# Optimization experiments

Measured on AMD Instinct MI355X. Metric: run time of the kernel, lower is better.

The kernel has to match this reference:

```python
import jax, jax.numpy as jnp
import numpy as np

D_MODEL, D_STATE, D_CONV, EXPAND = 1024, 16, 4, 2
D_INNER = EXPAND * D_MODEL            # 2048
DT_RANK = D_MODEL // 16               # 64
B, L = 2, 4096


def setup_inputs() -> dict:
    key = jax.random.key(0)
    ks = jax.random.split(key, 8)
    s = 0.02
    u = jax.random.normal(ks[0], (B, L, D_MODEL), jnp.float32)
    in_proj_w = jax.random.normal(ks[1], (2 * D_INNER, D_MODEL), jnp.float32) * s
    conv_w = jax.random.normal(ks[2], (D_INNER, D_CONV), jnp.float32) * 0.2
    conv_b = jnp.zeros((D_INNER,), jnp.float32)
    x_proj_w = jax.random.normal(ks[3], (DT_RANK + 2 * D_STATE, D_INNER), jnp.float32) * s
    dt_proj_w = jax.random.normal(ks[4], (D_INNER, DT_RANK), jnp.float32) * (DT_RANK ** -0.5)
    # dt bias initialized so softplus(dt_bias) in [1e-3, 1e-1], as in mamba-ssm
    dt = jnp.exp(jax.random.uniform(ks[5], (D_INNER,)) * (np.log(0.1) - np.log(1e-3)) + np.log(1e-3))
    dt_bias = jnp.log(-jnp.expm1(-dt) * jnp.exp(dt))  # inverse softplus
    A_log = jnp.log(jnp.tile(jnp.arange(1, D_STATE + 1, dtype=jnp.float32), (D_INNER, 1)))
    D_in = jnp.ones((D_INNER,), jnp.float32)
    out_proj_w = jax.random.normal(ks[6], (D_MODEL, D_INNER), jnp.float32) * s
    D_skip = jnp.ones((D_MODEL,), jnp.float32)
    return dict(u=u, in_proj_w=in_proj_w, conv_w=conv_w, conv_b=conv_b,
                x_proj_w=x_proj_w, dt_proj_w=dt_proj_w, dt_bias=dt_bias,
                A_log=A_log, D_in=D_in, out_proj_w=out_proj_w, D_skip=D_skip)


def _mamba(u, in_proj_w, conv_w, conv_b, x_proj_w, dt_proj_w, dt_bias,
           A_log, D_in, out_proj_w):
    b, l, _ = u.shape
    xz = jnp.einsum('bld,ed->ble', u, in_proj_w)      # (B,L,2*Din)
    x, z = jnp.split(xz, 2, axis=-1)
    # causal depthwise conv1d over time, kernel size D_CONV
    xp = jnp.pad(x, ((0, 0), (D_CONV - 1, 0), (0, 0)))
    x = sum(xp[:, k:k + l, :] * conv_w[:, k] for k in range(D_CONV)) + conv_b
    x = jax.nn.silu(x)
    x_dbl = jnp.einsum('bld,ed->ble', x, x_proj_w)    # (B,L,dt_rank+2N)
    dt = jax.nn.softplus(x_dbl[..., :DT_RANK] @ dt_proj_w.T + dt_bias)  # (B,L,Din)
    Bm = x_dbl[..., DT_RANK:DT_RANK + D_STATE]        # (B,L,N)
    Cm = x_dbl[..., DT_RANK + D_STATE:]               # (B,L,N)
    A = -jnp.exp(A_log)                               # (Din,N)

    def step(h, inp):
        dt_t, B_t, C_t, x_t = inp                     # (B,Din),(B,N),(B,N),(B,Din)
        dA = jnp.exp(dt_t[..., None] * A)             # (B,Din,N)
        h = dA * h + (dt_t * x_t)[..., None] * B_t[:, None, :]
        y = jnp.einsum('bdn,bn->bd', h, C_t)
        return h, y

    h0 = jnp.zeros((b, D_INNER, D_STATE), u.dtype)
    xs = (dt.transpose(1, 0, 2), Bm.transpose(1, 0, 2),
          Cm.transpose(1, 0, 2), x.transpose(1, 0, 2))
    _, ys = jax.lax.scan(step, h0, xs)                # (L,B,Din)
    y = ys.transpose(1, 0, 2) + x * D_in
    y = y * jax.nn.silu(z)
    return jnp.einsum('bld,ed->ble', y, out_proj_w)   # (B,L,D_MODEL)


def reference(u, in_proj_w, conv_w, conv_b, x_proj_w, dt_proj_w, dt_bias,
              A_log, D_in, out_proj_w, D_skip):
    y = _mamba(u, in_proj_w, conv_w, conv_b, x_proj_w, dt_proj_w, dt_bias,
               A_log, D_in, out_proj_w)
    return y + D_skip[None, None, :] * u
```

## Files before the change

kernel.cpp:

```cpp
#include <hip/hip_runtime.h>

typedef unsigned short u16;
typedef unsigned int u32;
typedef __attribute__((ext_vector_type(8))) short s16x8;
typedef __attribute__((ext_vector_type(4))) float f32x4;

__device__ inline u16 f2bf(float f){
    u32 u = __float_as_uint(f);
    u32 r = (u + 0x7fffu + ((u >> 16) & 1u)) >> 16;
    return (u16)r;
}
__device__ inline float bf2f(u16 h){
    return __uint_as_float(((u32)h) << 16);
}

#define GLOAD_LDS16(g, l) __builtin_amdgcn_global_load_lds( \
    (__attribute__((address_space(1))) void*)(void*)(g),    \
    (__attribute__((address_space(3))) void*)(l), 16, 0, 0)

#define MEMFENCE asm volatile("" ::: "memory")

__global__ __launch_bounds__(512, 2) void gemm256_in(
    const u16* __restrict__ A, const u16* __restrict__ B,
    int K, int nbn, u16* __restrict__ Cb, u16* __restrict__ Cb2)
{
    __shared__ u16 lds[2][2][256 * 64];
    const int tid  = threadIdx.x;
    const int lane = tid & 63, wave = tid >> 6;
    const int wr = wave >> 2, wc = wave & 3;
    const int l16 = lane & 15, lg = lane >> 4;

    int wgid = blockIdx.x, nwg = gridDim.x;
    int swz = wgid;
    if ((nwg & 7) == 0) { int cpx = nwg >> 3; swz = (wgid & 7) * cpx + (wgid >> 3); }
    const int bm = swz / nbn, bn = swz % nbn;

    const u16* Ab = A + (size_t)bm * 256 * K;
    const u16* Bb = B + (size_t)bn * 256 * K;

    const int srow   = wave * 8 + (lane >> 3);
    const int scol16 = (lane & 7) ^ ((lane >> 3) & 7);

    auto stageA = [&](int buf, int kt) {
        #pragma unroll
        for (int j = 0; j < 4; j++)
            GLOAD_LDS16(Ab + (size_t)(j * 64 + srow) * K + kt + scol16 * 8,
                        &lds[buf][0][(j * 64 + wave * 8) * 64]);
    };
    auto stageB = [&](int buf, int kt) {
        #pragma unroll
        for (int j = 0; j < 4; j++)
            GLOAD_LDS16(Bb + (size_t)(j * 64 + srow) * K + kt + scol16 * 8,
                        &lds[buf][1][(j * 64 + wave * 8) * 64]);
    };

    f32x4 acc[2][2][4][2] = {};
    s16x8 a[4][2], b0[2][2], b1[2][2];

    auto readA = [&](int buf, int mh) {
        #pragma unroll
        for (int m = 0; m < 4; m++)
            #pragma unroll
            for (int ks = 0; ks < 2; ks++) {
                int row = wr * 128 + mh * 64 + m * 16 + l16;
                int c16 = (ks * 4 + lg) ^ (l16 & 7);
                a[m][ks] = *(const s16x8*)&lds[buf][0][row * 64 + c16 * 8];
            }
    };
    auto readB = [&](int buf, int nh, s16x8 (&b)[2][2]) {
        #pragma unroll
        for (int n = 0; n < 2; n++)
            #pragma unroll
            for (int ks = 0; ks < 2; ks++) {
                int row = wc * 64 + nh * 32 + n * 16 + l16;
                int c16 = (ks * 4 + lg) ^ (l16 & 7);
                b[n][ks] = *(const s16x8*)&lds[buf][1][row * 64 + c16 * 8];
            }
    };

    const int NT = K >> 6;

    stageA(0, 0); stageB(0, 0);
    asm volatile("s_waitcnt vmcnt(0)" ::: "memory");
    __builtin_amdgcn_s_barrier();
    MEMFENCE;

    for (int t = 0; t < NT; t++) {
        const int bufc = t & 1;
        const bool pre = (t < NT - 1);
        #pragma unroll
        for (int p = 0; p < 4; p++) {
            const int mh = (p >> 1) & 1;
            const int nh = (p == 0 || p == 3) ? 0 : 1;
            if (p == 0 && pre) stageA(bufc ^ 1, (t + 1) << 6);
            if (p == 1 && pre) stageB(bufc ^ 1, (t + 1) << 6);
            if (p == 0) { readA(bufc, 0); readB(bufc, 0, b0); }
            if (p == 1) { readB(bufc, 1, b1); }
            if (p == 2) { readA(bufc, 1); }
            if (p == 3 && pre)
                asm volatile("s_waitcnt vmcnt(0)" ::: "memory");
            MEMFENCE;
            __builtin_amdgcn_s_barrier();
            MEMFENCE;
            __builtin_amdgcn_s_setprio(1);
            {
                s16x8 (&bb)[2][2] = (nh == 0) ? b0 : b1;
                #pragma unroll
                for (int m = 0; m < 4; m++)
                    #pragma unroll
                    for (int n = 0; n < 2; n++)
                        #pragma unroll
                        for (int ks = 0; ks < 2; ks++)
                            acc[mh][nh][m][n] = __builtin_amdgcn_mfma_f32_16x16x32_bf16(
                                a[m][ks], bb[n][ks], acc[mh][nh][m][n], 0, 0, 0);
            }
            __builtin_amdgcn_s_setprio(0);
            if (p == 3) {
                MEMFENCE;
                __builtin_amdgcn_s_barrier();
                MEMFENCE;
            }
        }
    }

    #pragma unroll
    for (int mh = 0; mh < 2; mh++)
        #pragma unroll
        for (int nh = 0; nh < 2; nh++)
            #pragma unroll
            for (int m = 0; m < 4; m++)
                #pragma unroll
                for (int n = 0; n < 2; n++) {
                    const int col = bn * 256 + wc * 64 + nh * 32 + n * 16 + l16;
                    #pragma unroll
                    for (int r = 0; r < 4; r++) {
                        const int row = bm * 256 + wr * 128 + mh * 64 + m * 16 + lg * 4 + r;
                        float v = acc[mh][nh][m][n][r];
                        if (col < 2048) Cb[(size_t)row * 2048 + col] = f2bf(v);
                        else            Cb2[(size_t)row * 2048 + (col - 2048)] = f2bf(v);
                    }
                }
}

__global__ __launch_bounds__(256) void gemm_out(
    const u16* __restrict__ A, const u16* __restrict__ B,
    int N, int K, int nbn,
    float* __restrict__ Cf, const float* __restrict__ aux0,
    const float* __restrict__ aux1)
{
    constexpr int BK = 64;
    __shared__ u16 As[128 * BK];
    __shared__ u16 Bs[128 * BK];
    const int tid  = threadIdx.x;
    const int lane = tid & 63, wave = tid >> 6;
    const int wr = wave >> 1, wc = wave & 1;
    const int l16 = lane & 15, lg = lane >> 4;

    int wgid = blockIdx.x, nwg = gridDim.x;
    int swz = wgid;
    if ((nwg & 7) == 0) { int cpx = nwg >> 3; swz = (wgid & 7) * cpx + (wgid >> 3); }
    const int bm = swz / nbn, bn = swz % nbn;

    const u16* Ab = A + (size_t)bm * 128 * K;
    const u16* Bb = B + (size_t)bn * 128 * K;

    f32x4 acc[4][4] = {};

    for (int kt = 0; kt < K; kt += BK) {
        #pragma unroll
        for (int p = 0; p < 4; p++) {
            int flat = (p * 256 + tid) * 8;
            int r = flat >> 6, c = flat & 63;
            GLOAD_LDS16(Ab + (size_t)r * K + kt + c, As + flat);
        }
        #pragma unroll
        for (int p = 0; p < 4; p++) {
            int flat = (p * 256 + tid) * 8;
            int r = flat >> 6, c = flat & 63;
            GLOAD_LDS16(Bb + (size_t)r * K + kt + c, Bs + flat);
        }
        asm volatile("s_waitcnt vmcnt(0)" ::: "memory");
        __syncthreads();
        #pragma unroll
        for (int kk = 0; kk < 2; kk++) {
            s16x8 a[4], b[4];
            #pragma unroll
            for (int m = 0; m < 4; m++)
                a[m] = *(const s16x8*)&As[(wr * 64 + m * 16 + l16) * BK + kk * 32 + lg * 8];
            #pragma unroll
            for (int n = 0; n < 4; n++)
                b[n] = *(const s16x8*)&Bs[(wc * 64 + n * 16 + l16) * BK + kk * 32 + lg * 8];
            #pragma unroll
            for (int m = 0; m < 4; m++)
                #pragma unroll
                for (int n = 0; n < 4; n++)
                    acc[m][n] = __builtin_amdgcn_mfma_f32_16x16x32_bf16(a[m], b[n], acc[m][n], 0, 0, 0);
        }
        __syncthreads();
    }

    const int row0 = bm * 128 + wr * 64 + lg * 4;
    const int col0 = bn * 128 + wc * 64 + l16;
    #pragma unroll
    for (int m = 0; m < 4; m++)
        #pragma unroll
        for (int n = 0; n < 4; n++) {
            const int col = col0 + n * 16;
            #pragma unroll
            for (int r = 0; r < 4; r++) {
                const int row = row0 + m * 16 + r;
                float o = acc[m][n][r] + aux0[col] * aux1[(size_t)row * N + col];
                Cf[(size_t)row * N + col] = o;
            }
        }
}

__global__ __launch_bounds__(256) void gemm_dt(
    const u16* __restrict__ A, const u16* __restrict__ B,
    int M, int N, int K,
    u16* __restrict__ Cb, const float* __restrict__ aux0)
{
    constexpr int BK = 64;
    __shared__ u16 As[128 * BK];
    __shared__ u16 Bs[128 * BK];
    const int tid  = threadIdx.x;
    const int lane = tid & 63, wave = tid >> 6;
    const int wr = wave >> 1, wc = wave & 1;
    const int bm = blockIdx.x, bn = blockIdx.y;
    const int l16 = lane & 15, lg = lane >> 4;

    const u16* Ab = A + (size_t)bm * 128 * K;
    const u16* Bb = B + (size_t)bn * 128 * K;

    f32x4 acc[4][4] = {};

    for (int kt = 0; kt < K; kt += BK) {
        #pragma unroll
        for (int p = 0; p < 4; p++) {
            int flat = (p * 256 + tid) * 8;
            int r = flat >> 6, c = flat & 63;
            GLOAD_LDS16(Ab + (size_t)r * K + kt + c, As + flat);
        }
        #pragma unroll
        for (int p = 0; p < 4; p++) {
            int flat = (p * 256 + tid) * 8;
            int r = flat >> 6, c = flat & 63;
            GLOAD_LDS16(Bb + (size_t)r * K + kt + c, Bs + flat);
        }
        asm volatile("s_waitcnt vmcnt(0)" ::: "memory");
        __syncthreads();
        #pragma unroll
        for (int kk = 0; kk < 2; kk++) {
            s16x8 a[4], b[4];
            #pragma unroll
            for (int m = 0; m < 4; m++)
                a[m] = *(const s16x8*)&As[(wr * 64 + m * 16 + l16) * BK + kk * 32 + lg * 8];
            #pragma unroll
            for (int n = 0; n < 4; n++)
                b[n] = *(const s16x8*)&Bs[(wc * 64 + n * 16 + l16) * BK + kk * 32 + lg * 8];
            #pragma unroll
            for (int m = 0; m < 4; m++)
                #pragma unroll
                for (int n = 0; n < 4; n++)
                    acc[m][n] = __builtin_amdgcn_mfma_f32_16x16x32_bf16(a[m], b[n], acc[m][n], 0, 0, 0);
        }
        __syncthreads();
    }

    const int row0 = bm * 128 + wr * 64 + lg * 4;
    const int col0 = bn * 128 + wc * 64 + l16;
    #pragma unroll
    for (int m = 0; m < 4; m++)
        #pragma unroll
        for (int n = 0; n < 4; n++) {
            const int col = col0 + n * 16;
            #pragma unroll
            for (int r = 0; r < 4; r++) {
                const int row = row0 + m * 16 + r;
                float t2 = acc[m][n][r] + aux0[col];
                float sp = (t2 > 15.f) ? t2 : __logf(1.f + __expf(t2));
                Cb[(size_t)row * N + col] = f2bf(sp);
            }
        }
}

__global__ __launch_bounds__(256) void gemm_xproj_sk(
    const u16* __restrict__ A, const u16* __restrict__ B,
    float* __restrict__ part)
{
    constexpr int BK = 64, K = 2048;
    __shared__ u16 As[128 * BK];
    __shared__ u16 Bs[128 * BK];
    const int tid  = threadIdx.x;
    const int lane = tid & 63, wave = tid >> 6;
    const int wr = wave >> 1, wc = wave & 1;
    const int bm = blockIdx.x, sk = blockIdx.y;
    const int l16 = lane & 15, lg = lane >> 4;

    const u16* Ab = A + (size_t)bm * 128 * K;
    const u16* Bb = B;
    const int kt0 = sk * 256;

    f32x4 acc[4][4] = {};

    for (int kt = kt0; kt < kt0 + 256; kt += BK) {
        #pragma unroll
        for (int p = 0; p < 4; p++) {
            int flat = (p * 256 + tid) * 8;
            int r = flat >> 6, c = flat & 63;
            GLOAD_LDS16(Ab + (size_t)r * K + kt + c, As + flat);
        }
        #pragma unroll
        for (int p = 0; p < 4; p++) {
            int flat = (p * 256 + tid) * 8;
            int r = flat >> 6, c = flat & 63;
            GLOAD_LDS16(Bb + (size_t)r * K + kt + c, Bs + flat);
        }
        asm volatile("s_waitcnt vmcnt(0)" ::: "memory");
        __syncthreads();
        #pragma unroll
        for (int kk = 0; kk < 2; kk++) {
            s16x8 a[4], b[4];
            #pragma unroll
            for (int m = 0; m < 4; m++)
                a[m] = *(const s16x8*)&As[(wr * 64 + m * 16 + l16) * BK + kk * 32 + lg * 8];
            #pragma unroll
            for (int n = 0; n < 4; n++)
                b[n] = *(const s16x8*)&Bs[(wc * 64 + n * 16 + l16) * BK + kk * 32 + lg * 8];
            #pragma unroll
            for (int m = 0; m < 4; m++)
                #pragma unroll
                for (int n = 0; n < 4; n++)
                    acc[m][n] = __builtin_amdgcn_mfma_f32_16x16x32_bf16(a[m], b[n], acc[m][n], 0, 0, 0);
        }
        __syncthreads();
    }

    float* pb = part + (size_t)sk * 8192 * 128;
    const int row0 = bm * 128 + wr * 64 + lg * 4;
    const int col0 = wc * 64 + l16;
    #pragma unroll
    for (int m = 0; m < 4; m++)
        #pragma unroll
        for (int n = 0; n < 4; n++)
            #pragma unroll
            for (int r = 0; r < 4; r++)
                pb[(size_t)(row0 + m * 16 + r) * 128 + col0 + n * 16] = acc[m][n][r];
}

__global__ __launch_bounds__(256) void combine_xproj(
    const float* __restrict__ part, u16* __restrict__ dtin,
    float* __restrict__ xBC)
{
    const int gid = blockIdx.x * 256 + threadIdx.x;
    const int row = gid >> 7, col = gid & 127;
    float s = 0.f;
    #pragma unroll
    for (int sk = 0; sk < 8; sk++) s += part[(size_t)sk * 8192 * 128 + gid];
    if (col < 64)      dtin[(size_t)row * 64 + col] = f2bf(s);
    else if (col < 96) xBC[(size_t)row * 32 + (col - 64)] = s;
}

__global__ __launch_bounds__(256) void cvt_all(
    const float* __restrict__ u, const float* __restrict__ Wi,
    const float* __restrict__ Wo, const float* __restrict__ Wdt,
    const float* __restrict__ Wx,
    u16* __restrict__ u_bf, u16* __restrict__ Wi_bf, u16* __restrict__ Wo_bf,
    u16* __restrict__ Wdt_bf, u16* __restrict__ Wx_bf)
{
    size_t i = ((size_t)blockIdx.x * 256 + threadIdx.x) * 4;
    const size_t E0 = 8388608, E1 = E0 + 4194304, E2 = E1 + 2097152, E3 = E2 + 131072;
    f32x4 v;
    u16* dst;
    size_t off;
    if (i < E0)      { off = i;      v = *(const f32x4*)(u + off);   dst = u_bf + off; }
    else if (i < E1) { off = i - E0; v = *(const f32x4*)(Wi + off);  dst = Wi_bf + off; }
    else if (i < E2) { off = i - E1; v = *(const f32x4*)(Wo + off);  dst = Wo_bf + off; }
    else if (i < E3) { off = i - E2; v = *(const f32x4*)(Wdt + off); dst = Wdt_bf + off; }
    else {
        off = i - E3;
        size_t row = off >> 11;
        if (row < 96) v = *(const f32x4*)(Wx + off);
        else          v = (f32x4){0.f, 0.f, 0.f, 0.f};
        dst = Wx_bf + off;
    }
    ushort4 o;
    o.x = f2bf(v[0]); o.y = f2bf(v[1]); o.z = f2bf(v[2]); o.w = f2bf(v[3]);
    *(ushort4*)dst = o;
}

__global__ __launch_bounds__(256) void conv_silu(
    const u16* __restrict__ xzx, const float* __restrict__ cw,
    const float* __restrict__ cb, u16* __restrict__ xc)
{
    const int tid = threadIdx.x;
    const int d0 = tid * 8;
    const int t0 = blockIdx.x * 16;
    const int b  = blockIdx.y;
    float W0[8], W1[8], W2[8], W3[8], BI[8];
    #pragma unroll
    for (int j = 0; j < 8; j++) {
        f32x4 w = *(const f32x4*)(cw + (size_t)(d0 + j) * 4);
        W0[j] = w[0]; W1[j] = w[1]; W2[j] = w[2]; W3[j] = w[3];
        BI[j] = cb[d0 + j];
    }
    const u16* xp = xzx + (size_t)(b * 4096) * 2048 + d0;
    u16* op = xc + (size_t)(b * 4096) * 2048 + d0;

    float x0[8], x1[8], x2[8];
    #pragma unroll
    for (int j = 0; j < 8; j++) { x0[j] = 0.f; x1[j] = 0.f; x2[j] = 0.f; }
    if (t0 >= 3) {
        s16x8 v0 = *(const s16x8*)(xp + (size_t)(t0 - 3) * 2048);
        s16x8 v1 = *(const s16x8*)(xp + (size_t)(t0 - 2) * 2048);
        s16x8 v2 = *(const s16x8*)(xp + (size_t)(t0 - 1) * 2048);
        #pragma unroll
        for (int j = 0; j < 8; j++) {
            x0[j] = bf2f((u16)v0[j]); x1[j] = bf2f((u16)v1[j]); x2[j] = bf2f((u16)v2[j]);
        }
    }
    #pragma unroll
    for (int k = 0; k < 16; k++) {
        int t = t0 + k;
        s16x8 cv = *(const s16x8*)(xp + (size_t)t * 2048);
        s16x8 o;
        #pragma unroll
        for (int j = 0; j < 8; j++) {
            float c = bf2f((u16)cv[j]);
            float s = BI[j] + W0[j] * x0[j] + W1[j] * x1[j] + W2[j] * x2[j] + W3[j] * c;
            float v = s * __fdividef(1.f, 1.f + __expf(-s));
            o[j] = (short)f2bf(v);
            x0[j] = x1[j]; x1[j] = x2[j]; x2[j] = c;
        }
        *(s16x8*)(op + (size_t)t * 2048) = o;
    }
}

__global__ __launch_bounds__(256) void scan_p1(
    const u16* __restrict__ dtb, const u16* __restrict__ xc,
    const float* __restrict__ xBC, const float* __restrict__ A_log,
    u16* __restrict__ Aagg, u16* __restrict__ Bagg)
{
    __shared__ float Bsh[64][16];
    const int tid = threadIdx.x;
    const int d = blockIdx.x * 256 + tid;
    const int c = blockIdx.y, b = blockIdx.z;

    {
        int ti = tid >> 2, p = tid & 3;
        f32x4 bv = *(const f32x4*)(xBC + ((size_t)(b * 4096 + c * 64 + ti)) * 32 + p * 4);
        *(f32x4*)&Bsh[ti][p * 4] = bv;
    }
    __syncthreads();

    float Adn[16];
    #pragma unroll
    for (int q = 0; q < 4; q++) {
        f32x4 al = *(const f32x4*)(A_log + (size_t)d * 16 + q * 4);
        #pragma unroll
        for (int j = 0; j < 4; j++) Adn[q * 4 + j] = -__expf(al[j]);
    }

    const size_t base = (size_t)(b * 4096 + c * 64) * 2048 + d;
    const u16* dtp = dtb + base;
    const u16* xp  = xc  + base;

    float h[16];
    #pragma unroll
    for (int n = 0; n < 16; n++) h[n] = 0.f;
    float sumdt = 0.f;

    float dtv = bf2f(dtp[0]), xv = bf2f(xp[0]);
    for (int t = 0; t < 64; t++) {
        float ndt = 0.f, nx = 0.f;
        if (t < 63) { ndt = bf2f(dtp[(size_t)(t + 1) * 2048]); nx = bf2f(xp[(size_t)(t + 1) * 2048]); }
        float dtx = dtv * xv;
        sumdt += dtv;
        f32x4 B0 = *(const f32x4*)&Bsh[t][0];
        f32x4 B1 = *(const f32x4*)&Bsh[t][4];
        f32x4 B2 = *(const f32x4*)&Bsh[t][8];
        f32x4 B3 = *(const f32x4*)&Bsh[t][12];
        #pragma unroll
        for (int n = 0; n < 16; n++) {
            float Bv = (n < 4) ? B0[n] : (n < 8) ? B1[n - 4] : (n < 12) ? B2[n - 8] : B3[n - 12];
            float aa = __expf(Adn[n] * dtv);
            h[n] = fmaf(aa, h[n], dtx * Bv);
        }
        dtv = ndt; xv = nx;
    }

    const size_t abase = ((size_t)(b * 2048 + d) * 16) * 64 + c;
    #pragma unroll
    for (int n = 0; n < 16; n++) {
        Aagg[abase + (size_t)n * 64] = f2bf(__expf(Adn[n] * sumdt));
        Bagg[abase + (size_t)n * 64] = f2bf(h[n]);
    }
}

__global__ __launch_bounds__(256) void scan_p2(
    const u16* __restrict__ Aagg, u16* __restrict__ BaggH0)
{
    const int gid = blockIdx.x * 256 + threadIdx.x;
    const size_t base = (size_t)gid * 64;
    s16x8 Ar[8], Br[8];
    #pragma unroll
    for (int i = 0; i < 8; i++) {
        Ar[i] = *(const s16x8*)(Aagg + base + i * 8);
        Br[i] = *(const s16x8*)(BaggH0 + base + i * 8);
    }
    s16x8 Hr[8];
    float h = 0.f;
    #pragma unroll
    for (int i = 0; i < 8; i++) {
        #pragma unroll
        for (int j = 0; j < 8; j++) {
            float ac = bf2f((u16)Ar[i][j]);
            float bc = bf2f((u16)Br[i][j]);
            Hr[i][j] = (short)f2bf(h);
            h = fmaf(ac, h, bc);
        }
    }
    #pragma unroll
    for (int i = 0; i < 8; i++)
        *(s16x8*)(BaggH0 + base + i * 8) = Hr[i];
}

__global__ __launch_bounds__(256) void scan_p3(
    const u16* __restrict__ dtb, const u16* __restrict__ xc,
    const float* __restrict__ xBC, const float* __restrict__ A_log,
    const u16* __restrict__ H0, const u16* __restrict__ xzz,
    const float* __restrict__ D_in, u16* __restrict__ yy)
{
    __shared__ float BCs[64][32];
    const int tid = threadIdx.x;
    const int d = blockIdx.x * 256 + tid;
    const int c = blockIdx.y, b = blockIdx.z;

    {
        int ti = tid >> 2, p = tid & 3;
        const float* src = xBC + ((size_t)(b * 4096 + c * 64 + ti)) * 32 + p * 8;
        f32x4 v0 = *(const f32x4*)src;
        f32x4 v1 = *(const f32x4*)(src + 4);
        *(f32x4*)&BCs[ti][p * 8] = v0;
        *(f32x4*)&BCs[ti][p * 8 + 4] = v1;
    }
    __syncthreads();

    float Adn[16];
    #pragma unroll
    for (int q = 0; q < 4; q++) {
        f32x4 al = *(const f32x4*)(A_log + (size_t)d * 16 + q * 4);
        #pragma unroll
        for (int j = 0; j < 4; j++) Adn[q * 4 + j] = -__expf(al[j]);
    }
    const float Dd = D_in[d];

    float h[16];
    const size_t hbase = ((size_t)(b * 2048 + d) * 16) * 64 + c;
    #pragma unroll
    for (int n = 0; n < 16; n++) h[n] = bf2f(H0[hbase + (size_t)n * 64]);

    const size_t base = (size_t)(b * 4096 + c * 64) * 2048 + d;
    const u16* dtp = dtb + base;
    const u16* xp  = xc  + base;
    const u16* zp  = xzz + base;
    u16* yp = yy + base;

    float dtv = bf2f(dtp[0]), xv = bf2f(xp[0]), zv = bf2f(zp[0]);
    for (int t = 0; t < 64; t++) {
        float ndt = 0.f, nx = 0.f, nz = 0.f;
        if (t < 63) {
            ndt = bf2f(dtp[(size_t)(t + 1) * 2048]);
            nx  = bf2f(xp[(size_t)(t + 1) * 2048]);
            nz  = bf2f(zp[(size_t)(t + 1) * 2048]);
        }
        float dtx = dtv * xv;
        f32x4 B0 = *(const f32x4*)&BCs[t][0];
        f32x4 B1 = *(const f32x4*)&BCs[t][4];
        f32x4 B2 = *(const f32x4*)&BCs[t][8];
        f32x4 B3 = *(const f32x4*)&BCs[t][12];
        f32x4 C0 = *(const f32x4*)&BCs[t][16];
        f32x4 C1 = *(const f32x4*)&BCs[t][20];
        f32x4 C2 = *(const f32x4*)&BCs[t][24];
        f32x4 C3 = *(const f32x4*)&BCs[t][28];
        float y = 0.f;
        #pragma unroll
        for (int n = 0; n < 16; n++) {
            float Bv = (n < 4) ? B0[n] : (n < 8) ? B1[n - 4] : (n < 12) ? B2[n - 8] : B3[n - 12];
            float Cv = (n < 4) ? C0[n] : (n < 8) ? C1[n - 4] : (n < 12) ? C2[n - 8] : C3[n - 12];
            float aa = __expf(Adn[n] * dtv);
            h[n] = fmaf(aa, h[n], dtx * Bv);
            y = fmaf(h[n], Cv, y);
        }
        float sz = zv * __fdividef(1.f, 1.f + __expf(-zv));
        float val = fmaf(xv, Dd, y) * sz;
        yp[(size_t)t * 2048] = f2bf(val);
        dtv = ndt; xv = nx; zv = nz;
    }
}

extern "C" void kernel_launch(void* const* d_in, const int* in_sizes, int n_in,
                              void* d_out, int out_size, void* d_ws, size_t ws_size,
                              hipStream_t stream)
{
    const float* u       = (const float*)d_in[0];
    const float* Wi      = (const float*)d_in[1];
    const float* conv_w  = (const float*)d_in[2];
    const float* conv_b  = (const float*)d_in[3];
    const float* Wx      = (const float*)d_in[4];
    const float* Wdt     = (const float*)d_in[5];
    const float* dt_bias = (const float*)d_in[6];
    const float* A_log   = (const float*)d_in[7];
    const float* D_in_   = (const float*)d_in[8];
    const float* Wo      = (const float*)d_in[9];
    const float* D_skip  = (const float*)d_in[10];
    float* out = (float*)d_out;
    (void)in_sizes; (void)n_in; (void)out_size;

    const size_t MB = 1u << 20;
    char* ws = (char*)d_ws;
    u16*   xzx    = (u16*)(ws + 0);
    float* xpart  = (float*)(ws + 0);
    u16*   Aagg   = (u16*)(ws + 0);
    u16*   BaggH0 = (u16*)(ws + 8 * MB);
    u16*   xzz    = (u16*)(ws + 32 * MB);
    u16*   xc     = (u16*)(ws + 64 * MB);
    u16*   u_bf   = (u16*)(ws + 96 * MB);
    u16*   Wi_bf  = (u16*)(ws + 112 * MB);
    u16*   dtb    = (u16*)(ws + 96 * MB);
    u16*   Wx_bf  = (u16*)(ws + 128 * MB);
    u16*   Wdt_bf = (u16*)(ws + 128 * MB + 512 * 1024);
    u16*   yybuf  = (u16*)(ws + 128 * MB);
    float* xBC    = (float*)(ws + 160 * MB);
    u16*   dtin   = (u16*)(ws + 161 * MB);
    u16*   Wo_bf  = (u16*)(ws + 162 * MB);
    const size_t NEED = 166 * MB;
    if (ws_size < NEED) return;

    cvt_all<<<14720, 256, 0, stream>>>(u, Wi, Wo, Wdt, Wx,
                                       u_bf, Wi_bf, Wo_bf, Wdt_bf, Wx_bf);

    gemm256_in<<<512, 512, 0, stream>>>(u_bf, Wi_bf, 1024, 16, xzx, xzz);
    conv_silu<<<dim3(256, 2), 256, 0, stream>>>(xzx, conv_w, conv_b, xc);

    gemm_xproj_sk<<<dim3(64, 8), 256, 0, stream>>>(xc, Wx_bf, xpart);
    combine_xproj<<<4096, 256, 0, stream>>>(xpart, dtin, xBC);

    gemm_dt<<<dim3(64, 16), 256, 0, stream>>>(dtin, Wdt_bf, 8192, 2048, 64,
                                              dtb, dt_bias);

    scan_p1<<<dim3(8, 64, 2), 256, 0, stream>>>(dtb, xc, xBC, A_log, Aagg, BaggH0);
    scan_p2<<<256, 256, 0, stream>>>(Aagg, BaggH0);
    scan_p3<<<dim3(8, 64, 2), 256, 0, stream>>>(dtb, xc, xBC, A_log, BaggH0, xzz,
                                                D_in_, yybuf);

    gemm_out<<<512, 256, 0, stream>>>(yybuf, Wo_bf, 1024, 2048, 8,
                                      out, D_skip, u);
}
```

Baseline: 387.3 us.

## Pipeline in-proj GEMM with half-tile staging and reuse 256 tile for out-proj

Adds a new in-projection GEMM that stages A and B in half tiles across two K buffers. Global-to-LDS loads for the next slices are interleaved with four MFMA phases per K step, separated by barriers and priority hints, and the LDS reads use an XOR swizzle. The old 256x256 kernel is repurposed for the output projection with the skip-connection epilogue, replacing the 128x128 gemm_out. The aim is to overlap memory traffic with matrix math and to reuse more data per tile on the out-proj. In exchange, occupancy drops to 1 block per CU for the in-proj, and out-proj runs only 128 workgroups, which may underfill the GPU.

```diff
diff --git a/kernel.cpp b/kernel.cpp
--- a/kernel.cpp
+++ b/kernel.cpp
@@ -19,10 +19,145 @@
     (__attribute__((address_space(3))) void*)(l), 16, 0, 0)
 
 #define MEMFENCE asm volatile("" ::: "memory")
-
-__global__ __launch_bounds__(512, 2) void gemm256_in(
+#define BAR do { MEMFENCE; __builtin_amdgcn_s_barrier(); MEMFENCE; } while (0)
+
+__global__ __launch_bounds__(512, 1) void gemm256_pipe(
     const u16* __restrict__ A, const u16* __restrict__ B,
     int K, int nbn, u16* __restrict__ Cb, u16* __restrict__ Cb2)
+{
+    __shared__ u16 lds[2][2][2][128 * 64];
+    const int tid  = threadIdx.x;
+    const int lane = tid & 63, wave = tid >> 6;
+    const int wr = wave >> 2, wc = wave & 3;
+    const int l16 = lane & 15, lg = lane >> 4;
+
+    int wgid = blockIdx.x, nwg = gridDim.x;
+    int swz = wgid;
+    if ((nwg & 7) == 0) { int cpx = nwg >> 3; swz = (wgid & 7) * cpx + (wgid >> 3); }
+    const int bm = swz / nbn, bn = swz % nbn;
+
+    const u16* Ab = A + (size_t)bm * 256 * K;
+    const u16* Bb = B + (size_t)bn * 256 * K;
+
+    auto stage_half = [&](int kbuf, int mat, int half, int kt) {
+        const u16* src = mat ? Bb : Ab;
+        #pragma unroll
+        for (int j = 0; j < 2; j++) {
+            int slot = j * 512 + tid;
+            int r = slot >> 3, cg = slot & 7;
+            GLOAD_LDS16(src + (size_t)(half * 128 + r) * K + kt + ((cg ^ (r & 7)) << 3),
+                        &lds[kbuf][mat][half][(j * 512 + wave * 64) * 8]);
+        }
+    };
+
+    f32x4 acc[2][2][4][2] = {};
+    s16x8 a[4][2], b0[2][2], b1[2][2];
+
+    auto readA = [&](int kbuf, int mh) {
+        #pragma unroll
+        for (int m = 0; m < 4; m++)
+            #pragma unroll
+            for (int ks = 0; ks < 2; ks++) {
+                int r = mh * 64 + m * 16 + l16;
+                int cg = (ks * 4 + lg) ^ (l16 & 7);
+                a[m][ks] = *(const s16x8*)&lds[kbuf][0][wr][r * 64 + cg * 8];
+            }
+    };
+    auto readB = [&](int kbuf, int nh, s16x8 (&bb)[2][2]) {
+        #pragma unroll
+        for (int n = 0; n < 2; n++)
+            #pragma unroll
+            for (int ks = 0; ks < 2; ks++) {
+                int row = wc * 64 + nh * 32 + n * 16 + l16;
+                int half = row >> 7, r = row & 127;
+                int cg = (ks * 4 + lg) ^ (l16 & 7);
+                bb[n][ks] = *(const s16x8*)&lds[kbuf][1][half][r * 64 + cg * 8];
+            }
+    };
+    auto PH = [&](int mh, int nh, s16x8 (&bb)[2][2]) {
+        BAR;
+        __builtin_amdgcn_s_setprio(1);
+        #pragma unroll
+        for (int m = 0; m < 4; m++)
+            #pragma unroll
+            for (int n = 0; n < 2; n++)
+                #pragma unroll
+                for (int ks = 0; ks < 2; ks++)
+                    acc[mh][nh][m][n] = __builtin_amdgcn_mfma_f32_16x16x32_bf16(
+                        a[m][ks], bb[n][ks], acc[mh][nh][m][n], 0, 0, 0);
+        __builtin_amdgcn_s_setprio(0);
+        BAR;
+    };
+
+    const int NT = K >> 6;
+
+    stage_half(0, 1, 0, 0); stage_half(0, 1, 1, 0);
+    stage_half(0, 0, 0, 0); stage_half(0, 0, 1, 0);
+    stage_half(1, 1, 0, 64);
+    stage_half(1, 0, 0, 64); stage_half(1, 0, 1, 64);
+    asm volatile("s_waitcnt vmcnt(6)" ::: "memory");
+    BAR;
+
+    for (int it = 0; it < (NT >> 1); it++) {
+        const int t1k = (2 * it + 1) << 6;
+        const int t2k = (2 * it + 2) << 6;
+        const int t3k = (2 * it + 3) << 6;
+        const bool pre = (2 * it + 2) < NT;
+        readA(0, 0); readB(0, 0, b0);
+        stage_half(1, 1, 1, t1k);
+        PH(0, 0, b0);
+        readB(0, 1, b1);
+        PH(0, 1, b1);
+        readA(0, 1);
+        if (pre) stage_half(0, 1, 0, t2k);
+        PH(1, 1, b1);
+        if (pre) {
+            stage_half(0, 1, 1, t2k);
+            asm volatile("s_waitcnt vmcnt(4)" ::: "memory");
+        } else {
+            asm volatile("s_waitcnt vmcnt(0)" ::: "memory");
+        }
+        PH(1, 0, b0);
+        readA(1, 0); readB(1, 0, b0);
+        if (pre) stage_half(0, 0, 0, t2k);
+        PH(0, 0, b0);
+        readB(1, 1, b1);
+        if (pre) stage_half(0, 0, 1, t2k);
+        PH(0, 1, b1);
+        readA(1, 1);
+        if (pre) stage_half(1, 1, 0, t3k);
+        PH(1, 1, b1);
+        if (pre) {
+            stage_half(1, 0, 0, t3k); stage_half(1, 0, 1, t3k);
+            asm volatile("s_waitcnt vmcnt(6)" ::: "memory");
+        }
+        PH(1, 0, b0);
+    }
+
+    #pragma unroll
+    for (int mh = 0; mh < 2; mh++)
+        #pragma unroll
+        for (int nh = 0; nh < 2; nh++)
+            #pragma unroll
+            for (int m = 0; m < 4; m++)
+                #pragma unroll
+                for (int n = 0; n < 2; n++) {
+                    const int col = bn * 256 + wc * 64 + nh * 32 + n * 16 + l16;
+                    #pragma unroll
+                    for (int r = 0; r < 4; r++) {
+                        const int row = bm * 256 + wr * 128 + mh * 64 + m * 16 + lg * 4 + r;
+                        float v = acc[mh][nh][m][n][r];
+                        if (col < 2048) Cb[(size_t)row * 2048 + col] = f2bf(v);
+                        else            Cb2[(size_t)row * 2048 + (col - 2048)] = f2bf(v);
+                    }
+                }
+}
+
+__global__ __launch_bounds__(512, 2) void gemm256_out(
+    const u16* __restrict__ A, const u16* __restrict__ B,
+    int N, int K, int nbn,
+    float* __restrict__ Cf, const float* __restrict__ aux0,
+    const float* __restrict__ aux1)
 {
     __shared__ u16 lds[2][2][256 * 64];
     const int tid  = threadIdx.x;
@@ -135,84 +270,10 @@
                     #pragma unroll
                     for (int r = 0; r < 4; r++) {
                         const int row = bm * 256 + wr * 128 + mh * 64 + m * 16 + lg * 4 + r;
-                        float v = acc[mh][nh][m][n][r];
-                        if (col < 2048) Cb[(size_t)row * 2048 + col] = f2bf(v);
-                        else            Cb2[(size_t)row * 2048 + (col - 2048)] = f2bf(v);
+                        float o = acc[mh][nh][m][n][r] + aux0[col] * aux1[(size_t)row * N + col];
+                        Cf[(size_t)row * N + col] = o;
                     }
                 }
-}
-
-__global__ __launch_bounds__(256) void gemm_out(
-    const u16* __restrict__ A, const u16* __restrict__ B,
-    int N, int K, int nbn,
-    float* __restrict__ Cf, const float* __restrict__ aux0,
-    const float* __restrict__ aux1)
-{
-    constexpr int BK = 64;
-    __shared__ u16 As[128 * BK];
-    __shared__ u16 Bs[128 * BK];
-    const int tid  = threadIdx.x;
-    const int lane = tid & 63, wave = tid >> 6;
-    const int wr = wave >> 1, wc = wave & 1;
-    const int l16 = lane & 15, lg = lane >> 4;
-
-    int wgid = blockIdx.x, nwg = gridDim.x;
-    int swz = wgid;
-    if ((nwg & 7) == 0) { int cpx = nwg >> 3; swz = (wgid & 7) * cpx + (wgid >> 3); }
-    const int bm = swz / nbn, bn = swz % nbn;
-
-    const u16* Ab = A + (size_t)bm * 128 * K;
-    const u16* Bb = B + (size_t)bn * 128 * K;
-
-    f32x4 acc[4][4] = {};
-
-    for (int kt = 0; kt < K; kt += BK) {
-        #pragma unroll
-        for (int p = 0; p < 4; p++) {
-            int flat = (p * 256 + tid) * 8;
-            int r = flat >> 6, c = flat & 63;
-            GLOAD_LDS16(Ab + (size_t)r * K + kt + c, As + flat);
-        }
-        #pragma unroll
-        for (int p = 0; p < 4; p++) {
-            int flat = (p * 256 + tid) * 8;
-            int r = flat >> 6, c = flat & 63;
-            GLOAD_LDS16(Bb + (size_t)r * K + kt + c, Bs + flat);
-        }
-        asm volatile("s_waitcnt vmcnt(0)" ::: "memory");
-        __syncthreads();
-        #pragma unroll
-        for (int kk = 0; kk < 2; kk++) {
-            s16x8 a[4], b[4];
-            #pragma unroll
-            for (int m = 0; m < 4; m++)
-                a[m] = *(const s16x8*)&As[(wr * 64 + m * 16 + l16) * BK + kk * 32 + lg * 8];
-            #pragma unroll
-            for (int n = 0; n < 4; n++)
-                b[n] = *(const s16x8*)&Bs[(wc * 64 + n * 16 + l16) * BK + kk * 32 + lg * 8];
-            #pragma unroll
-            for (int m = 0; m < 4; m++)
-                #pragma unroll
-                for (int n = 0; n < 4; n++)
-                    acc[m][n] = __builtin_amdgcn_mfma_f32_16x16x32_bf16(a[m], b[n], acc[m][n], 0, 0, 0);
-        }
-        __syncthreads();
-    }
-
-    const int row0 = bm * 128 + wr * 64 + lg * 4;
-    const int col0 = bn * 128 + wc * 64 + l16;
-    #pragma unroll
-    for (int m = 0; m < 4; m++)
-        #pragma unroll
-        for (int n = 0; n < 4; n++) {
-            const int col = col0 + n * 16;
-            #pragma unroll
-            for (int r = 0; r < 4; r++) {
-                const int row = row0 + m * 16 + r;
-                float o = acc[m][n][r] + aux0[col] * aux1[(size_t)row * N + col];
-                Cf[(size_t)row * N + col] = o;
-            }
-        }
 }
 
 __global__ __launch_bounds__(256) void gemm_dt(
@@ -640,7 +701,7 @@
     cvt_all<<<14720, 256, 0, stream>>>(u, Wi, Wo, Wdt, Wx,
                                        u_bf, Wi_bf, Wo_bf, Wdt_bf, Wx_bf);
 
-    gemm256_in<<<512, 512, 0, stream>>>(u_bf, Wi_bf, 1024, 16, xzx, xzz);
+    gemm256_pipe<<<512, 512, 0, stream>>>(u_bf, Wi_bf, 1024, 16, xzx, xzz);
     conv_silu<<<dim3(256, 2), 256, 0, stream>>>(xzx, conv_w, conv_b, xc);
 
     gemm_xproj_sk<<<dim3(64, 8), 256, 0, stream>>>(xc, Wx_bf, xpart);
@@ -654,6 +715,6 @@
     scan_p3<<<dim3(8, 64, 2), 256, 0, stream>>>(dtb, xc, xBC, A_log, BaggH0, xzz,
                                                 D_in_, yybuf);
 
-    gemm_out<<<512, 256, 0, stream>>>(yybuf, Wo_bf, 1024, 2048, 8,
-                                      out, D_skip, u);
-}
+    gemm256_out<<<128, 512, 0, stream>>>(yybuf, Wo_bf, 1024, 2048, 4,
+                                         out, D_skip, u);
+}
```

Result: no change. 382.0 us (-1.4%).

## Replace out-projection GEMM with 256x256 split-K pipelined kernel plus combine

Applied to the files above, without the earlier changes.

The output projection GEMM moves from 128x128 single-buffered tiles to a 256x256 tile kernel with double-buffered, XOR-swizzled LDS staging and interleaved MFMA phases. K is split in two so the grid still has 256 workgroups, and each half writes fp32 partials. A separate elementwise kernel adds the partials and the D_skip*u residual. This trades a per-K-step sync stall and lower tile reuse for extra partial-sum traffic (two 32MB fp32 buffers) and one more kernel launch.

```diff
diff --git a/kernel.cpp b/kernel.cpp
--- a/kernel.cpp
+++ b/kernel.cpp
@@ -142,77 +142,143 @@
                 }
 }
 
-__global__ __launch_bounds__(256) void gemm_out(
+__global__ __launch_bounds__(512, 2) void gemm256_psk(
     const u16* __restrict__ A, const u16* __restrict__ B,
-    int N, int K, int nbn,
-    float* __restrict__ Cf, const float* __restrict__ aux0,
-    const float* __restrict__ aux1)
-{
-    constexpr int BK = 64;
-    __shared__ u16 As[128 * BK];
-    __shared__ u16 Bs[128 * BK];
+    float* __restrict__ p0, float* __restrict__ p1)
+{
+    constexpr int LDA = 2048, NT = 16;
+    __shared__ u16 lds[2][2][256 * 64];
     const int tid  = threadIdx.x;
     const int lane = tid & 63, wave = tid >> 6;
-    const int wr = wave >> 1, wc = wave & 1;
+    const int wr = wave >> 2, wc = wave & 3;
     const int l16 = lane & 15, lg = lane >> 4;
 
     int wgid = blockIdx.x, nwg = gridDim.x;
     int swz = wgid;
     if ((nwg & 7) == 0) { int cpx = nwg >> 3; swz = (wgid & 7) * cpx + (wgid >> 3); }
-    const int bm = swz / nbn, bn = swz % nbn;
-
-    const u16* Ab = A + (size_t)bm * 128 * K;
-    const u16* Bb = B + (size_t)bn * 128 * K;
-
-    f32x4 acc[4][4] = {};
-
-    for (int kt = 0; kt < K; kt += BK) {
+    const int sk = swz >> 7;
+    const int tile = swz & 127;
+    const int bm = tile >> 2, bn = tile & 3;
+    const int kt0 = sk << 10;
+
+    const u16* Ab = A + (size_t)bm * 256 * LDA + kt0;
+    const u16* Bb = B + (size_t)bn * 256 * LDA + kt0;
+    float* P = sk ? p1 : p0;
+
+    const int srow   = wave * 8 + (lane >> 3);
+    const int scol16 = (lane & 7) ^ ((lane >> 3) & 7);
+
+    auto stageA = [&](int buf, int kt) {
+        #pragma unroll
+        for (int j = 0; j < 4; j++)
+            GLOAD_LDS16(Ab + (size_t)(j * 64 + srow) * LDA + kt + scol16 * 8,
+                        &lds[buf][0][(j * 64 + wave * 8) * 64]);
+    };
+    auto stageB = [&](int buf, int kt) {
+        #pragma unroll
+        for (int j = 0; j < 4; j++)
+            GLOAD_LDS16(Bb + (size_t)(j * 64 + srow) * LDA + kt + scol16 * 8,
+                        &lds[buf][1][(j * 64 + wave * 8) * 64]);
+    };
+
+    f32x4 acc[2][2][4][2] = {};
+    s16x8 a[4][2], b0[2][2], b1[2][2];
+
+    auto readA = [&](int buf, int mh) {
+        #pragma unroll
+        for (int m = 0; m < 4; m++)
+            #pragma unroll
+            for (int ks = 0; ks < 2; ks++) {
+                int row = wr * 128 + mh * 64 + m * 16 + l16;
+                int c16 = (ks * 4 + lg) ^ (l16 & 7);
+                a[m][ks] = *(const s16x8*)&lds[buf][0][row * 64 + c16 * 8];
+            }
+    };
+    auto readB = [&](int buf, int nh, s16x8 (&b)[2][2]) {
+        #pragma unroll
+        for (int n = 0; n < 2; n++)
+            #pragma unroll
+            for (int ks = 0; ks < 2; ks++) {
+                int row = wc * 64 + nh * 32 + n * 16 + l16;
+                int c16 = (ks * 4 + lg) ^ (l16 & 7);
+                b[n][ks] = *(const s16x8*)&lds[buf][1][row * 64 + c16 * 8];
+            }
+    };
+
+    stageA(0, 0); stageB(0, 0);
+    asm volatile("s_waitcnt vmcnt(0)" ::: "memory");
+    __builtin_amdgcn_s_barrier();
+    MEMFENCE;
+
+    for (int t = 0; t < NT; t++) {
+        const int bufc = t & 1;
+        const bool pre = (t < NT - 1);
         #pragma unroll
         for (int p = 0; p < 4; p++) {
-            int flat = (p * 256 + tid) * 8;
-            int r = flat >> 6, c = flat & 63;
-            GLOAD_LDS16(Ab + (size_t)r * K + kt + c, As + flat);
-        }
-        #pragma unroll
-        for (int p = 0; p < 4; p++) {
-            int flat = (p * 256 + tid) * 8;
-            int r = flat >> 6, c = flat & 63;
-            GLOAD_LDS16(Bb + (size_t)r * K + kt + c, Bs + flat);
-        }
-        asm volatile("s_waitcnt vmcnt(0)" ::: "memory");
-        __syncthreads();
-        #pragma unroll
-        for (int kk = 0; kk < 2; kk++) {
-            s16x8 a[4], b[4];
-            #pragma unroll
-            for (int m = 0; m < 4; m++)
-                a[m] = *(const s16x8*)&As[(wr * 64 + m * 16 + l16) * BK + kk * 32 + lg * 8];
-            #pragma unroll
-            for (int n = 0; n < 4; n++)
-                b[n] = *(const s16x8*)&Bs[(wc * 64 + n * 16 + l16) * BK + kk * 32 + lg * 8];
+            const int mh = (p >> 1) & 1;
+            const int nh = (p == 0 || p == 3) ? 0 : 1;
+            if (p == 0 && pre) stageA(bufc ^ 1, (t + 1) << 6);
+            if (p == 1 && pre) stageB(bufc ^ 1, (t + 1) << 6);
+            if (p == 0) { readA(bufc, 0); readB(bufc, 0, b0); }
+            if (p == 1) { readB(bufc, 1, b1); }
+            if (p == 2) { readA(bufc, 1); }
+            if (p == 3 && pre)
+                asm volatile("s_waitcnt vmcnt(0)" ::: "memory");
+            MEMFENCE;
+            __builtin_amdgcn_s_barrier();
+            MEMFENCE;
+            __builtin_amdgcn_s_setprio(1);
+            {
+                s16x8 (&bb)[2][2] = (nh == 0) ? b0 : b1;
+                #pragma unroll
+                for (int m = 0; m < 4; m++)
+                    #pragma unroll
+                    for (int n = 0; n < 2; n++)
+                        #pragma unroll
+                        for (int ks = 0; ks < 2; ks++)
+                            acc[mh][nh][m][n] = __builtin_amdgcn_mfma_f32_16x16x32_bf16(
+                                a[m][ks], bb[n][ks], acc[mh][nh][m][n], 0, 0, 0);
+            }
+            __builtin_amdgcn_s_setprio(0);
+            if (p == 3) {
+                MEMFENCE;
+                __builtin_amdgcn_s_barrier();
+                MEMFENCE;
+            }
+        }
+    }
+
+    #pragma unroll
+    for (int mh = 0; mh < 2; mh++)
+        #pragma unroll
+        for (int nh = 0; nh < 2; nh++)
             #pragma unroll
             for (int m = 0; m < 4; m++)
                 #pragma unroll
-                for (int n = 0; n < 4; n++)
-                    acc[m][n] = __builtin_amdgcn_mfma_f32_16x16x32_bf16(a[m], b[n], acc[m][n], 0, 0, 0);
-        }
-        __syncthreads();
-    }
-
-    const int row0 = bm * 128 + wr * 64 + lg * 4;
-    const int col0 = bn * 128 + wc * 64 + l16;
-    #pragma unroll
-    for (int m = 0; m < 4; m++)
-        #pragma unroll
-        for (int n = 0; n < 4; n++) {
-            const int col = col0 + n * 16;
-            #pragma unroll
-            for (int r = 0; r < 4; r++) {
-                const int row = row0 + m * 16 + r;
-                float o = acc[m][n][r] + aux0[col] * aux1[(size_t)row * N + col];
-                Cf[(size_t)row * N + col] = o;
-            }
-        }
+                for (int n = 0; n < 2; n++) {
+                    const int col = bn * 256 + wc * 64 + nh * 32 + n * 16 + l16;
+                    #pragma unroll
+                    for (int r = 0; r < 4; r++) {
+                        const int row = bm * 256 + wr * 128 + mh * 64 + m * 16 + lg * 4 + r;
+                        P[(size_t)row * 1024 + col] = acc[mh][nh][m][n][r];
+                    }
+                }
+}
+
+__global__ __launch_bounds__(256) void combine_out(
+    const float* __restrict__ p0, const float* __restrict__ p1,
+    const float* __restrict__ u, const float* __restrict__ D_skip,
+    float* __restrict__ out)
+{
+    const int i = (blockIdx.x * 256 + threadIdx.x) * 4;
+    f32x4 a = *(const f32x4*)(p0 + i);
+    f32x4 b = *(const f32x4*)(p1 + i);
+    f32x4 uu = *(const f32x4*)(u + i);
+    f32x4 ds = *(const f32x4*)(D_skip + (i & 1023));
+    f32x4 o;
+    #pragma unroll
+    for (int j = 0; j < 4; j++) o[j] = a[j] + b[j] + ds[j] * uu[j];
+    *(f32x4*)(out + i) = o;
 }
 
 __global__ __launch_bounds__(256) void gemm_dt(
@@ -622,8 +688,10 @@
     u16*   xzx    = (u16*)(ws + 0);
     float* xpart  = (float*)(ws + 0);
     u16*   Aagg   = (u16*)(ws + 0);
+    float* pout0  = (float*)(ws + 0);
     u16*   BaggH0 = (u16*)(ws + 8 * MB);
     u16*   xzz    = (u16*)(ws + 32 * MB);
+    float* pout1  = (float*)(ws + 32 * MB);
     u16*   xc     = (u16*)(ws + 64 * MB);
     u16*   u_bf   = (u16*)(ws + 96 * MB);
     u16*   Wi_bf  = (u16*)(ws + 112 * MB);
@@ -654,6 +722,6 @@
     scan_p3<<<dim3(8, 64, 2), 256, 0, stream>>>(dtb, xc, xBC, A_log, BaggH0, xzz,
                                                 D_in_, yybuf);
 
-    gemm_out<<<512, 256, 0, stream>>>(yybuf, Wo_bf, 1024, 2048, 8,
-                                      out, D_skip, u);
-}
+    gemm256_psk<<<256, 512, 0, stream>>>(yybuf, Wo_bf, pout0, pout1);
+    combine_out<<<8192, 256, 0, stream>>>(pout0, pout1, u, D_skip, out);
+}
```

Measured after the change: 384.2 us. No clear change (-0.8%).
